# Performance work log

Hardware: AMD Instinct MI355X
Metric: run time of the kernel (lower is better)

The kernel has to match this reference:

```python
import jax, jax.numpy as jnp
import numpy as np

N_EMBED = 512
HEAD = 64
N_HEADS = N_EMBED // HEAD  # 8
N_LAYERS = 6
BLOCK = 2048
B = 4
T = 2048
SCALE = N_LAYERS / 3 ** (-0.25)  # = n_layers * 3**0.25, applied to q,k,v and FFN output


def setup_inputs() -> dict:
    key = jax.random.key(0)
    ks = jax.random.split(key, 8)
    sd = 1.0 / np.sqrt(N_EMBED)
    return {
        "x": jax.random.normal(ks[0], (B, T, N_EMBED), jnp.float32),
        "wq": jax.random.normal(ks[1], (N_HEADS, N_EMBED, HEAD), jnp.float32) * sd,
        "wk": jax.random.normal(ks[2], (N_HEADS, N_EMBED, HEAD), jnp.float32) * sd,
        "wv": jax.random.normal(ks[3], (N_HEADS, N_EMBED, HEAD), jnp.float32) * sd,
        "w_proj": jax.random.normal(ks[4], (N_EMBED, N_EMBED), jnp.float32) * sd,
        "b_proj": jnp.zeros((N_EMBED,), jnp.float32),
        "w1": jax.random.normal(ks[5], (N_EMBED, 4 * N_EMBED), jnp.float32) * sd,
        "b1": jnp.zeros((4 * N_EMBED,), jnp.float32),
        "w2": jax.random.normal(ks[6], (4 * N_EMBED, N_EMBED), jnp.float32) / np.sqrt(4 * N_EMBED),
        "b2": jnp.zeros((N_EMBED,), jnp.float32),
        "g1": jnp.ones((N_EMBED,), jnp.float32),
        "be1": jnp.zeros((N_EMBED,), jnp.float32),
        "g2": jnp.ones((N_EMBED,), jnp.float32),
        "be2": jnp.zeros((N_EMBED,), jnp.float32),
    }


def _layernorm(x, g, b, eps=1e-5):
    mu = jnp.mean(x, axis=-1, keepdims=True)
    var = jnp.var(x, axis=-1, keepdims=True)
    return (x - mu) * jax.lax.rsqrt(var + eps) * g + b


def _attention(x, wq, wk, wv, w_proj, b_proj):
    # x: [B,T,C]; wq/wk/wv: [H,C,D]  (vectorized over the per-head Linears)
    q = jnp.einsum("btc,hcd->bhtd", x, wq) * SCALE
    k = jnp.einsum("btc,hcd->bhtd", x, wk) * SCALE
    v = jnp.einsum("btc,hcd->bhtd", x, wv) * SCALE
    # NOTE: original scales by C**-0.5 where C = n_embed (input dim), not head_size
    wei = jnp.einsum("bhtd,bhsd->bhts", q, k) * (N_EMBED ** -0.5)
    causal = jnp.tril(jnp.ones((T, T), bool))  # tril buffer, sliced to [T,T]
    wei = jnp.where(causal, wei, -jnp.inf)
    wei = jax.nn.softmax(wei, axis=-1)
    out = jnp.einsum("bhts,bhsd->bhtd", wei, v)
    out = out.transpose(0, 2, 1, 3).reshape(x.shape)  # concat heads on last dim
    return out @ w_proj + b_proj


def _feedforward(x, w1, b1, w2, b2):
    h = jax.nn.relu(x @ w1 + b1)
    return (h @ w2 + b2) * SCALE


def reference(x, wq, wk, wv, w_proj, b_proj, w1, b1, w2, b2, g1, be1, g2, be2):
    x = x + _attention(_layernorm(x, g1, be1), wq, wk, wv, w_proj, b_proj)
    x = x + _feedforward(_layernorm(x, g2, be2), w1, b1, w2, b2)
    return x
```

## Files before the change

kernel.cpp:

```cpp
#include <hip/hip_runtime.h>

typedef _Float16 f16;
typedef f16 f16x4 __attribute__((ext_vector_type(4)));
typedef f16 f16x8 __attribute__((ext_vector_type(8)));
typedef float f32x4 __attribute__((ext_vector_type(4)));

#define AS1 __attribute__((address_space(1)))
#define AS3 __attribute__((address_space(3)))

constexpr float kScale  = 7.896444077714954f;
constexpr float kScaleQ = (float)(7.896444077714954 / 22.627416997969522 * 1.4426950408889634);

__device__ __forceinline__ void g2l16(const void* g, void* l) {
  __builtin_amdgcn_global_load_lds((const AS1 void*)g, (AS3 void*)l, 16, 0, 0);
}

__device__ __forceinline__ void ln_body(
    const float* __restrict__ x, const float* __restrict__ g,
    const float* __restrict__ be, f16* __restrict__ out, int rowblk) {
  int row = rowblk * 4 + ((int)threadIdx.x >> 6);
  int lane = threadIdx.x & 63;
  const float* xr = x + (size_t)row * 512;
  float xa[8];
  *(float4*)&xa[0] = *(const float4*)(xr + lane * 8);
  *(float4*)&xa[4] = *(const float4*)(xr + lane * 8 + 4);
  float s = 0.f, q = 0.f;
#pragma unroll
  for (int i = 0; i < 8; ++i) { s += xa[i]; q += xa[i] * xa[i]; }
#pragma unroll
  for (int off = 32; off; off >>= 1) { s += __shfl_xor(s, off); q += __shfl_xor(q, off); }
  float mean = s * (1.f / 512.f);
  float var = q * (1.f / 512.f) - mean * mean;
  float rstd = rsqrtf(var + 1e-5f);
  float ga[8], ba[8];
  *(float4*)&ga[0] = *(const float4*)(g + lane * 8);
  *(float4*)&ga[4] = *(const float4*)(g + lane * 8 + 4);
  *(float4*)&ba[0] = *(const float4*)(be + lane * 8);
  *(float4*)&ba[4] = *(const float4*)(be + lane * 8 + 4);
  f16x8 o;
#pragma unroll
  for (int i = 0; i < 8; ++i) o[i] = (f16)((xa[i] - mean) * rstd * ga[i] + ba[i]);
  *(f16x8*)(out + (size_t)row * 512 + lane * 8) = o;
}

__global__ __launch_bounds__(256) void ln_kernel(
    const float* __restrict__ x, const float* __restrict__ g,
    const float* __restrict__ be, f16* __restrict__ out) {
  ln_body(x, g, be, out, blockIdx.x);
}

__global__ __launch_bounds__(256) void preproc_kernel(
    const float* __restrict__ wq, const float* __restrict__ wk,
    const float* __restrict__ wv, const float* __restrict__ wp,
    const float* __restrict__ w1, const float* __restrict__ w2,
    const float* __restrict__ x, const float* __restrict__ g1,
    const float* __restrict__ be1,
    f16* __restrict__ Wqkv, f16* __restrict__ Wp, f16* __restrict__ W1t,
    f16* __restrict__ W2t, f16* __restrict__ x_ln) {
  int bid = blockIdx.x;
  if (bid >= 3072) { ln_body(x, g1, be1, x_ln, bid - 3072); return; }
  __shared__ float t[32][33];
  const float* in; f16* out; int R, Cc, bx, by, bz = 0; float scale;
  if (bid < 768) {
    int which = bid >> 8, rem = bid & 255;
    bx = rem & 1; by = (rem >> 1) & 15; bz = rem >> 5;
    in = which == 0 ? wq : (which == 1 ? wk : wv);
    out = Wqkv + (size_t)which * 512 * 512;
    R = 512; Cc = 64; scale = which == 0 ? kScaleQ : kScale;
  } else if (bid < 1024) {
    int rem = bid - 768; bx = rem & 15; by = rem >> 4;
    in = wp; out = Wp; R = 512; Cc = 512; scale = 1.f;
  } else if (bid < 2048) {
    int rem = bid - 1024; bx = rem & 63; by = rem >> 6;
    in = w1; out = W1t; R = 512; Cc = 2048; scale = 1.f;
  } else {
    int rem = bid - 2048; bx = rem & 15; by = rem >> 4;
    in = w2; out = W2t; R = 2048; Cc = 512; scale = kScale;
  }
  const float* im = in + (size_t)bz * R * Cc;
  f16* om = out + (size_t)bz * Cc * R;
  int c0 = bx * 32, r0 = by * 32;
  int tx = threadIdx.x & 31, ty = threadIdx.x >> 5;
#pragma unroll
  for (int i = 0; i < 4; ++i) {
    int rr = ty + i * 8;
    t[rr][tx] = im[(size_t)(r0 + rr) * Cc + c0 + tx] * scale;
  }
  __syncthreads();
#pragma unroll
  for (int i = 0; i < 4; ++i) {
    int rr = ty + i * 8;
    om[(size_t)(c0 + rr) * R + r0 + tx] = (f16)t[tx][rr];
  }
}

template <int MODE, bool W8>
__global__ __launch_bounds__(W8 ? 512 : 256) void gemm_bt(
    const f16* __restrict__ A, const f16* __restrict__ Bt,
    const float* __restrict__ bias, const float* __restrict__ res,
    float* __restrict__ outf, f16* __restrict__ outb,
    f16* __restrict__ qo, f16* __restrict__ ko, f16* __restrict__ vo,
    int N, int K) {
  __shared__ f16 lA[2][128 * 64], lB[2][128 * 64];
  constexpr int NF = W8 ? 2 : 4;
  constexpr int WCW = W8 ? 32 : 64;
  int tid = threadIdx.x;
  int lane = tid & 63, w = tid >> 6;
  int wr = W8 ? (w >> 2) : (w >> 1);
  int wc = W8 ? (w & 3) : (w & 1);
  int gq = lane >> 4, r = lane & 15;
  int m0 = blockIdx.x * 128, n0 = blockIdx.y * 128;
  size_t Kb = (size_t)K * 2;
  const char* Ab = (const char*)A + (size_t)m0 * Kb;
  const char* Bb = (const char*)Bt + (size_t)n0 * Kb;
  f32x4 acc[4][NF] = {};
  int srow = lane >> 3, sslot = lane & 7;
  auto stage = [&](int buf, int kt) {
#pragma unroll
    for (int i = 0; i < (W8 ? 2 : 4); ++i) {
      int chunk = i * (W8 ? 8 : 4) + w;
      int row = chunk * 8 + srow;
      int slot = sslot ^ (row & 7);
      g2l16(Ab + (size_t)row * Kb + kt * 2 + slot * 16, (char*)lA + buf * 16384 + chunk * 1024);
      g2l16(Bb + (size_t)row * Kb + kt * 2 + slot * 16, (char*)lB + buf * 16384 + chunk * 1024);
    }
  };
  stage(0, 0);
  int cur = 0;
  for (int kt = 0; kt < K; kt += 64) {
    __syncthreads();
    if (kt + 64 < K) stage(cur ^ 1, kt + 64);
    const char* bA = (const char*)lA + cur * 16384;
    const char* bB = (const char*)lB + cur * 16384;
    f16x8 af[4][2], bfr[NF][2];
#pragma unroll
    for (int f = 0; f < 4; ++f)
#pragma unroll
      for (int ks = 0; ks < 2; ++ks) {
        int ra = wr * 64 + f * 16 + r;
        af[f][ks] = *(const f16x8*)(bA + ra * 128 + (((ks * 4 + gq) ^ (ra & 7)) * 16));
      }
#pragma unroll
    for (int fn = 0; fn < NF; ++fn)
#pragma unroll
      for (int ks = 0; ks < 2; ++ks) {
        int rb = wc * WCW + fn * 16 + r;
        bfr[fn][ks] = *(const f16x8*)(bB + rb * 128 + (((ks * 4 + gq) ^ (rb & 7)) * 16));
      }
    __builtin_amdgcn_s_setprio(1);
#pragma unroll
    for (int fm = 0; fm < 4; ++fm)
#pragma unroll
      for (int fn = 0; fn < NF; ++fn)
#pragma unroll
        for (int ks = 0; ks < 2; ++ks)
          acc[fm][fn] = __builtin_amdgcn_mfma_f32_16x16x32_f16(af[fm][ks], bfr[fn][ks], acc[fm][fn], 0, 0, 0);
    __builtin_amdgcn_s_setprio(0);
    cur ^= 1;
  }
#pragma unroll
  for (int fm = 0; fm < 4; ++fm)
#pragma unroll
    for (int fn = 0; fn < NF; ++fn)
#pragma unroll
      for (int rg = 0; rg < 4; ++rg) {
        int row = m0 + wr * 64 + fm * 16 + gq * 4 + rg;
        int col = n0 + wc * WCW + fn * 16 + r;
        float v = acc[fm][fn][rg];
        if constexpr (MODE == 1) {
          outf[(size_t)row * N + col] = v + bias[col] + res[(size_t)row * N + col];
        } else if constexpr (MODE == 2) {
          outb[(size_t)row * N + col] = (f16)fmaxf(v + bias[col], 0.f);
        } else if constexpr (MODE == 3) {
          outf[(size_t)row * N + col] = v + bias[col] * kScale + res[(size_t)row * N + col];
        } else {
          int bb = row >> 11, t = row & 2047;
          int which = col >> 9, hd = col & 511, hh = hd >> 6, d = hd & 63;
          size_t bh = (size_t)bb * 8 + hh;
          if (which == 0)      qo[(bh * 2048 + t) * 64 + d] = (f16)v;
          else if (which == 1) ko[(bh * 2048 + t) * 64 + d] = (f16)v;
          else                 vo[(bh * 64 + d) * 2048 + t] = (f16)v;
        }
      }
}

__global__ __launch_bounds__(256) void attn_kernel(
    const f16* __restrict__ Q, const f16* __restrict__ K,
    const f16* __restrict__ Vt, f16* __restrict__ out) {
  __shared__ f16 lK[2][64 * 64], lV[2][64 * 64];
  __shared__ f16 lP[4][16 * 72];
  int tid = threadIdx.x, lane = tid & 63, w = tid >> 6;
  int gq = lane >> 4, r = lane & 15;
  int bh = blockIdx.x;
  int p = blockIdx.y;
  const char* Qb = (const char*)(Q + (size_t)bh * 2048 * 64);
  const char* Kb = (const char*)(K + (size_t)bh * 2048 * 64);
  const char* Vb = (const char*)(Vt + (size_t)bh * 64 * 2048);
  int q0A = p * 64 + w * 16;
  int q0B = (31 - p) * 64 + w * 16;
  f16x8 qfA[2], qfB[2];
#pragma unroll
  for (int ks = 0; ks < 2; ++ks) {
    qfA[ks] = *(const f16x8*)(Qb + (size_t)(q0A + r) * 128 + ks * 64 + gq * 16);
    qfB[ks] = *(const f16x8*)(Qb + (size_t)(q0B + r) * 128 + ks * 64 + gq * 16);
  }
  f16x8 ones;
#pragma unroll
  for (int i = 0; i < 8; ++i) ones[i] = (f16)1.f;
  f32x4 OA[4] = {}, OB[4] = {}, OlA = {}, OlB = {};
  float mA = -1e30f, mB = -1e30f;
  int srow = lane >> 3, sslot = lane & 7;

  auto stage = [&](int buf, int kv) {
    int j0 = kv * 64;
#pragma unroll
    for (int i = 0; i < 2; ++i) {
      int chunk = i * 4 + w;
      int row = chunk * 8 + srow;
      int slot = sslot ^ (row & 7);
      g2l16(Kb + (size_t)(j0 + row) * 128 + slot * 16, (char*)lK + buf * 8192 + chunk * 1024);
      g2l16(Vb + (size_t)row * 4096 + j0 * 2 + slot * 16, (char*)lV + buf * 8192 + chunk * 1024);
    }
  };

  f16x8 vf[4][2];
  auto smpv = [&](f32x4 (&s)[4], float& m, f32x4 (&O)[4], f32x4& Ol) {
    float t0 = fmaxf(fmaxf(s[0][0], s[0][1]), fmaxf(s[0][2], s[0][3]));
    float t1 = fmaxf(fmaxf(s[1][0], s[1][1]), fmaxf(s[1][2], s[1][3]));
    float t2 = fmaxf(fmaxf(s[2][0], s[2][1]), fmaxf(s[2][2], s[2][3]));
    float t3 = fmaxf(fmaxf(s[3][0], s[3][1]), fmaxf(s[3][2], s[3][3]));
    float pmax = fmaxf(fmaxf(t0, t1), fmaxf(t2, t3));
    pmax = fmaxf(pmax, __shfl_xor(pmax, 16));
    pmax = fmaxf(pmax, __shfl_xor(pmax, 32));
    float mn = fmaxf(m, pmax);
    if (mn - m > 11.5f) {
      float sc = exp2f(m - mn);
#pragma unroll
      for (int fd = 0; fd < 4; ++fd) O[fd] *= sc;
      Ol *= sc;
      m = mn;
    } else {
      mn = m;
    }
#pragma unroll
    for (int fc = 0; fc < 4; ++fc) {
      f16x4 pv;
#pragma unroll
      for (int rg = 0; rg < 4; ++rg) pv[rg] = (f16)exp2f(s[fc][rg] - mn);
      *(f16x4*)((char*)&lP[w][0] + r * 144 + fc * 32 + gq * 8) = pv;
    }
    f16x8 pf[2];
#pragma unroll
    for (int ks = 0; ks < 2; ++ks)
      pf[ks] = *(const f16x8*)((const char*)&lP[w][0] + r * 144 + ks * 64 + gq * 16);
#pragma unroll
    for (int fd = 0; fd < 4; ++fd)
#pragma unroll
      for (int ks = 0; ks < 2; ++ks)
        O[fd] = __builtin_amdgcn_mfma_f32_16x16x32_f16(vf[fd][ks], pf[ks], O[fd], 0, 0, 0);
#pragma unroll
    for (int ks = 0; ks < 2; ++ks)
      Ol = __builtin_amdgcn_mfma_f32_16x16x32_f16(ones, pf[ks], Ol, 0, 0, 0);
  };

  int nkv = 32 - p;
  stage(0, 0);
  int cur = 0;
  for (int kv = 0; kv < nkv; ++kv) {
    int j0 = kv * 64;
    __syncthreads();
    if (kv + 1 < nkv) stage(cur ^ 1, kv + 1);
    const char* bK = (const char*)lK + cur * 8192;
    const char* bV = (const char*)lV + cur * 8192;
    f16x8 kf[4][2];
#pragma unroll
    for (int fc = 0; fc < 4; ++fc)
#pragma unroll
      for (int ks = 0; ks < 2; ++ks) {
        int rj = fc * 16 + r;
        kf[fc][ks] = *(const f16x8*)(bK + rj * 128 + (((ks * 4 + gq) ^ (rj & 7)) * 16));
      }
#pragma unroll
    for (int fd = 0; fd < 4; ++fd)
#pragma unroll
      for (int ks = 0; ks < 2; ++ks) {
        int rd = fd * 16 + r;
        vf[fd][ks] = *(const f16x8*)(bV + rd * 128 + (((ks * 4 + gq) ^ (rd & 7)) * 16));
      }
    f32x4 sB[4] = {};
#pragma unroll
    for (int ks = 0; ks < 2; ++ks)
#pragma unroll
      for (int fc = 0; fc < 4; ++fc)
        sB[fc] = __builtin_amdgcn_mfma_f32_16x16x32_f16(kf[fc][ks], qfB[ks], sB[fc], 0, 0, 0);
    if (kv == nkv - 1) {
      int t = q0B + r;
#pragma unroll
      for (int fc = 0; fc < 4; ++fc)
#pragma unroll
        for (int rg = 0; rg < 4; ++rg) {
          int j = j0 + fc * 16 + gq * 4 + rg;
          if (j > t) sB[fc][rg] = -1e30f;
        }
    }
    smpv(sB, mB, OB, OlB);
    if (kv <= p) {
      f32x4 sA[4] = {};
#pragma unroll
      for (int ks = 0; ks < 2; ++ks)
#pragma unroll
        for (int fc = 0; fc < 4; ++fc)
          sA[fc] = __builtin_amdgcn_mfma_f32_16x16x32_f16(kf[fc][ks], qfA[ks], sA[fc], 0, 0, 0);
      if (kv == p) {
        int t = q0A + r;
#pragma unroll
        for (int fc = 0; fc < 4; ++fc)
#pragma unroll
          for (int rg = 0; rg < 4; ++rg) {
            int j = j0 + fc * 16 + gq * 4 + rg;
            if (j > t) sA[fc][rg] = -1e30f;
          }
      }
      smpv(sA, mA, OA, OlA);
    }
    cur ^= 1;
  }
  int bb = bh >> 3, hh = bh & 7;
  auto wout = [&](int q0, f32x4 (&O)[4], float l) {
    float inv = 1.f / l;
    int t = q0 + r;
    f16* o = out + ((size_t)bb * 2048 + t) * 512 + hh * 64 + gq * 4;
#pragma unroll
    for (int fd = 0; fd < 4; ++fd) {
      f16x4 v;
#pragma unroll
      for (int rg = 0; rg < 4; ++rg) v[rg] = (f16)(O[fd][rg] * inv);
      *(f16x4*)(o + fd * 16) = v;
    }
  };
  wout(q0A, OA, OlA[0]);
  wout(q0B, OB, OlB[0]);
}

extern "C" void kernel_launch(void* const* d_in, const int* in_sizes, int n_in,
                              void* d_out, int out_size, void* d_ws, size_t ws_size,
                              hipStream_t stream) {
  (void)in_sizes; (void)n_in; (void)out_size; (void)ws_size;
  const float* x      = (const float*)d_in[0];
  const float* wq     = (const float*)d_in[1];
  const float* wk     = (const float*)d_in[2];
  const float* wv     = (const float*)d_in[3];
  const float* w_proj = (const float*)d_in[4];
  const float* b_proj = (const float*)d_in[5];
  const float* w1     = (const float*)d_in[6];
  const float* b1     = (const float*)d_in[7];
  const float* w2     = (const float*)d_in[8];
  const float* b2     = (const float*)d_in[9];
  const float* g1     = (const float*)d_in[10];
  const float* be1    = (const float*)d_in[11];
  const float* g2     = (const float*)d_in[12];
  const float* be2    = (const float*)d_in[13];
  float* outp = (float*)d_out;

  char* ws = (char*)d_ws;
  size_t off = 0;
  auto alloc = [&](size_t bytes) {
    char* p = ws + off;
    off += (bytes + 255) & ~(size_t)255;
    return p;
  };
  const size_t MC2 = (size_t)8192 * 512 * 2;
  f16* x_ln  = (f16*)alloc(MC2);
  f16* qb    = (f16*)alloc(MC2);
  f16* kb    = (f16*)alloc(MC2);
  f16* vb    = (f16*)alloc(MC2);
  f16* attn  = (f16*)alloc(MC2);
  float* x1  = (float*)alloc((size_t)8192 * 512 * 4);
  f16* Wqkv  = (f16*)alloc((size_t)1536 * 512 * 2);
  f16* Wp    = (f16*)alloc((size_t)512 * 512 * 2);
  f16* W1t   = (f16*)alloc((size_t)2048 * 512 * 2);
  f16* W2t   = (f16*)alloc((size_t)512 * 2048 * 2);
  f16* x1_ln = x_ln;
  f16* hbuf  = qb;

  preproc_kernel<<<5120, 256, 0, stream>>>(wq, wk, wv, w_proj, w1, w2, x, g1, be1,
                                           Wqkv, Wp, W1t, W2t, x_ln);
  gemm_bt<0, false><<<dim3(64, 12), 256, 0, stream>>>(x_ln, Wqkv, nullptr, nullptr, nullptr, nullptr,
                                                      qb, kb, vb, 1536, 512);
  attn_kernel<<<dim3(32, 16), 256, 0, stream>>>(qb, kb, vb, attn);
  gemm_bt<1, true><<<dim3(64, 4), 512, 0, stream>>>(attn, Wp, b_proj, x, x1, nullptr,
                                                    nullptr, nullptr, nullptr, 512, 512);
  ln_kernel<<<2048, 256, 0, stream>>>(x1, g2, be2, x1_ln);
  gemm_bt<2, false><<<dim3(64, 16), 256, 0, stream>>>(x1_ln, W1t, b1, nullptr, nullptr, hbuf,
                                                      nullptr, nullptr, nullptr, 2048, 512);
  gemm_bt<3, true><<<dim3(64, 4), 512, 0, stream>>>(hbuf, W2t, b2, x1, outp, nullptr,
                                                    nullptr, nullptr, nullptr, 512, 2048);
}
```

Baseline: 165.9 us.

## Replace paired causal query tiles with one query tile per block, heaviest first

Measured after the change: 163.1 us. Within noise of the previous version (-1.7%).

```diff
diff --git a/kernel.cpp b/kernel.cpp
--- a/kernel.cpp
+++ b/kernel.cpp
@@ -192,23 +192,20 @@
   int tid = threadIdx.x, lane = tid & 63, w = tid >> 6;
   int gq = lane >> 4, r = lane & 15;
   int bh = blockIdx.x;
-  int p = blockIdx.y;
+  int qt = 31 - (int)blockIdx.y;
   const char* Qb = (const char*)(Q + (size_t)bh * 2048 * 64);
   const char* Kb = (const char*)(K + (size_t)bh * 2048 * 64);
   const char* Vb = (const char*)(Vt + (size_t)bh * 64 * 2048);
-  int q0A = p * 64 + w * 16;
-  int q0B = (31 - p) * 64 + w * 16;
-  f16x8 qfA[2], qfB[2];
-#pragma unroll
-  for (int ks = 0; ks < 2; ++ks) {
-    qfA[ks] = *(const f16x8*)(Qb + (size_t)(q0A + r) * 128 + ks * 64 + gq * 16);
-    qfB[ks] = *(const f16x8*)(Qb + (size_t)(q0B + r) * 128 + ks * 64 + gq * 16);
-  }
+  int q0 = qt * 64 + w * 16;
+  f16x8 qf[2];
+#pragma unroll
+  for (int ks = 0; ks < 2; ++ks)
+    qf[ks] = *(const f16x8*)(Qb + (size_t)(q0 + r) * 128 + ks * 64 + gq * 16);
   f16x8 ones;
 #pragma unroll
   for (int i = 0; i < 8; ++i) ones[i] = (f16)1.f;
-  f32x4 OA[4] = {}, OB[4] = {}, OlA = {}, OlB = {};
-  float mA = -1e30f, mB = -1e30f;
+  f32x4 O[4] = {}, Ol = {};
+  float m = -1e30f;
   int srow = lane >> 3, sslot = lane & 7;
 
   auto stage = [&](int buf, int kv) {
@@ -223,8 +220,41 @@
     }
   };
 
-  f16x8 vf[4][2];
-  auto smpv = [&](f32x4 (&s)[4], float& m, f32x4 (&O)[4], f32x4& Ol) {
+  int nkv = qt + 1;
+  stage(0, 0);
+  int cur = 0;
+  for (int kv = 0; kv < nkv; ++kv) {
+    int j0 = kv * 64;
+    __syncthreads();
+    if (kv + 1 < nkv) stage(cur ^ 1, kv + 1);
+    const char* bK = (const char*)lK + cur * 8192;
+    const char* bV = (const char*)lV + cur * 8192;
+    f16x8 kf[4][2], vf[4][2];
+#pragma unroll
+    for (int fc = 0; fc < 4; ++fc)
+#pragma unroll
+      for (int ks = 0; ks < 2; ++ks) {
+        int rj = fc * 16 + r;
+        int off = rj * 128 + (((ks * 4 + gq) ^ (rj & 7)) * 16);
+        kf[fc][ks] = *(const f16x8*)(bK + off);
+        vf[fc][ks] = *(const f16x8*)(bV + off);
+      }
+    f32x4 s[4] = {};
+#pragma unroll
+    for (int ks = 0; ks < 2; ++ks)
+#pragma unroll
+      for (int fc = 0; fc < 4; ++fc)
+        s[fc] = __builtin_amdgcn_mfma_f32_16x16x32_f16(kf[fc][ks], qf[ks], s[fc], 0, 0, 0);
+    if (kv == qt) {
+      int t = q0 + r;
+#pragma unroll
+      for (int fc = 0; fc < 4; ++fc)
+#pragma unroll
+        for (int rg = 0; rg < 4; ++rg) {
+          int j = j0 + fc * 16 + gq * 4 + rg;
+          if (j > t) s[fc][rg] = -1e30f;
+        }
+    }
     float t0 = fmaxf(fmaxf(s[0][0], s[0][1]), fmaxf(s[0][2], s[0][3]));
     float t1 = fmaxf(fmaxf(s[1][0], s[1][1]), fmaxf(s[1][2], s[1][3]));
     float t2 = fmaxf(fmaxf(s[2][0], s[2][1]), fmaxf(s[2][2], s[2][3]));
@@ -261,85 +291,19 @@
 #pragma unroll
     for (int ks = 0; ks < 2; ++ks)
       Ol = __builtin_amdgcn_mfma_f32_16x16x32_f16(ones, pf[ks], Ol, 0, 0, 0);
-  };
-
-  int nkv = 32 - p;
-  stage(0, 0);
-  int cur = 0;
-  for (int kv = 0; kv < nkv; ++kv) {
-    int j0 = kv * 64;
-    __syncthreads();
-    if (kv + 1 < nkv) stage(cur ^ 1, kv + 1);
-    const char* bK = (const char*)lK + cur * 8192;
-    const char* bV = (const char*)lV + cur * 8192;
-    f16x8 kf[4][2];
-#pragma unroll
-    for (int fc = 0; fc < 4; ++fc)
-#pragma unroll
-      for (int ks = 0; ks < 2; ++ks) {
-        int rj = fc * 16 + r;
-        kf[fc][ks] = *(const f16x8*)(bK + rj * 128 + (((ks * 4 + gq) ^ (rj & 7)) * 16));
-      }
-#pragma unroll
-    for (int fd = 0; fd < 4; ++fd)
-#pragma unroll
-      for (int ks = 0; ks < 2; ++ks) {
-        int rd = fd * 16 + r;
-        vf[fd][ks] = *(const f16x8*)(bV + rd * 128 + (((ks * 4 + gq) ^ (rd & 7)) * 16));
-      }
-    f32x4 sB[4] = {};
-#pragma unroll
-    for (int ks = 0; ks < 2; ++ks)
-#pragma unroll
-      for (int fc = 0; fc < 4; ++fc)
-        sB[fc] = __builtin_amdgcn_mfma_f32_16x16x32_f16(kf[fc][ks], qfB[ks], sB[fc], 0, 0, 0);
-    if (kv == nkv - 1) {
-      int t = q0B + r;
-#pragma unroll
-      for (int fc = 0; fc < 4; ++fc)
-#pragma unroll
-        for (int rg = 0; rg < 4; ++rg) {
-          int j = j0 + fc * 16 + gq * 4 + rg;
-          if (j > t) sB[fc][rg] = -1e30f;
-        }
-    }
-    smpv(sB, mB, OB, OlB);
-    if (kv <= p) {
-      f32x4 sA[4] = {};
-#pragma unroll
-      for (int ks = 0; ks < 2; ++ks)
-#pragma unroll
-        for (int fc = 0; fc < 4; ++fc)
-          sA[fc] = __builtin_amdgcn_mfma_f32_16x16x32_f16(kf[fc][ks], qfA[ks], sA[fc], 0, 0, 0);
-      if (kv == p) {
-        int t = q0A + r;
-#pragma unroll
-        for (int fc = 0; fc < 4; ++fc)
-#pragma unroll
-          for (int rg = 0; rg < 4; ++rg) {
-            int j = j0 + fc * 16 + gq * 4 + rg;
-            if (j > t) sA[fc][rg] = -1e30f;
-          }
-      }
-      smpv(sA, mA, OA, OlA);
-    }
     cur ^= 1;
   }
   int bb = bh >> 3, hh = bh & 7;
-  auto wout = [&](int q0, f32x4 (&O)[4], float l) {
-    float inv = 1.f / l;
-    int t = q0 + r;
-    f16* o = out + ((size_t)bb * 2048 + t) * 512 + hh * 64 + gq * 4;
-#pragma unroll
-    for (int fd = 0; fd < 4; ++fd) {
-      f16x4 v;
-#pragma unroll
-      for (int rg = 0; rg < 4; ++rg) v[rg] = (f16)(O[fd][rg] * inv);
-      *(f16x4*)(o + fd * 16) = v;
-    }
-  };
-  wout(q0A, OA, OlA[0]);
-  wout(q0B, OB, OlB[0]);
+  float inv = 1.f / Ol[0];
+  int t = q0 + r;
+  f16* o = out + ((size_t)bb * 2048 + t) * 512 + hh * 64 + gq * 4;
+#pragma unroll
+  for (int fd = 0; fd < 4; ++fd) {
+    f16x4 v;
+#pragma unroll
+    for (int rg = 0; rg < 4; ++rg) v[rg] = (f16)(O[fd][rg] * inv);
+    *(f16x4*)(o + fd * 16) = v;
+  }
 }
 
 extern "C" void kernel_launch(void* const* d_in, const int* in_sizes, int n_in,
@@ -387,7 +351,7 @@
                                            Wqkv, Wp, W1t, W2t, x_ln);
   gemm_bt<0, false><<<dim3(64, 12), 256, 0, stream>>>(x_ln, Wqkv, nullptr, nullptr, nullptr, nullptr,
                                                       qb, kb, vb, 1536, 512);
-  attn_kernel<<<dim3(32, 16), 256, 0, stream>>>(qb, kb, vb, attn);
+  attn_kernel<<<dim3(32, 32), 256, 0, stream>>>(qb, kb, vb, attn);
   gemm_bt<1, true><<<dim3(64, 4), 512, 0, stream>>>(attn, Wp, b_proj, x, x1, nullptr,
                                                     nullptr, nullptr, nullptr, 512, 512);
   ln_kernel<<<2048, 256, 0, stream>>>(x1, g2, be2, x1_ln);
```

## Pair adjacent query tiles per block, fold running max into MFMA accumulator init

Applied to the files above, without the earlier changes.

Result: slower. 185.3 us (+11.7%).

```diff
diff --git a/kernel.cpp b/kernel.cpp
--- a/kernel.cpp
+++ b/kernel.cpp
@@ -3,6 +3,7 @@
 typedef _Float16 f16;
 typedef f16 f16x4 __attribute__((ext_vector_type(4)));
 typedef f16 f16x8 __attribute__((ext_vector_type(8)));
+typedef __fp16 h16x2 __attribute__((ext_vector_type(2)));
 typedef float f32x4 __attribute__((ext_vector_type(4)));
 
 #define AS1 __attribute__((address_space(1)))
@@ -188,16 +189,17 @@
     const f16* __restrict__ Q, const f16* __restrict__ K,
     const f16* __restrict__ Vt, f16* __restrict__ out) {
   __shared__ f16 lK[2][64 * 64], lV[2][64 * 64];
-  __shared__ f16 lP[4][16 * 72];
+  __shared__ f16 lP[4][2][16 * 64];
   int tid = threadIdx.x, lane = tid & 63, w = tid >> 6;
   int gq = lane >> 4, r = lane & 15;
   int bh = blockIdx.x;
-  int p = blockIdx.y;
+  int qt = 15 - (int)blockIdx.y;
   const char* Qb = (const char*)(Q + (size_t)bh * 2048 * 64);
   const char* Kb = (const char*)(K + (size_t)bh * 2048 * 64);
   const char* Vb = (const char*)(Vt + (size_t)bh * 64 * 2048);
-  int q0A = p * 64 + w * 16;
-  int q0B = (31 - p) * 64 + w * 16;
+  int q0A = qt * 128 + w * 16;
+  int q0B = q0A + 64;
+  int dgA = 2 * qt, dgB = 2 * qt + 1;
   f16x8 qfA[2], qfB[2];
 #pragma unroll
   for (int ks = 0; ks < 2; ++ks) {
@@ -210,6 +212,7 @@
   f32x4 OA[4] = {}, OB[4] = {}, OlA = {}, OlB = {};
   float mA = -1e30f, mB = -1e30f;
   int srow = lane >> 3, sslot = lane & 7;
+  int swz = (r & 7) << 4;
 
   auto stage = [&](int buf, int kv) {
     int j0 = kv * 64;
@@ -223,36 +226,40 @@
     }
   };
 
-  f16x8 vf[4][2];
-  auto smpv = [&](f32x4 (&s)[4], float& m, f32x4 (&O)[4], f32x4& Ol) {
-    float t0 = fmaxf(fmaxf(s[0][0], s[0][1]), fmaxf(s[0][2], s[0][3]));
-    float t1 = fmaxf(fmaxf(s[1][0], s[1][1]), fmaxf(s[1][2], s[1][3]));
-    float t2 = fmaxf(fmaxf(s[2][0], s[2][1]), fmaxf(s[2][2], s[2][3]));
-    float t3 = fmaxf(fmaxf(s[3][0], s[3][1]), fmaxf(s[3][2], s[3][3]));
-    float pmax = fmaxf(fmaxf(t0, t1), fmaxf(t2, t3));
+  f16x8 kf[4][2], vf[4][2];
+  auto smpv = [&](f32x4 (&s)[4], float& m, f32x4 (&O)[4], f32x4& Ol, char* lPw) {
+    float pmax = s[0][0];
+#pragma unroll
+    for (int fc = 0; fc < 4; ++fc)
+#pragma unroll
+      for (int rg = 0; rg < 4; ++rg)
+        if (fc + rg) pmax = fmaxf(pmax, s[fc][rg]);
     pmax = fmaxf(pmax, __shfl_xor(pmax, 16));
     pmax = fmaxf(pmax, __shfl_xor(pmax, 32));
-    float mn = fmaxf(m, pmax);
-    if (mn - m > 11.5f) {
-      float sc = exp2f(m - mn);
+    if (pmax > 11.5f || m < -1e29f) {
+      float sc = exp2f(-pmax);
 #pragma unroll
       for (int fd = 0; fd < 4; ++fd) O[fd] *= sc;
       Ol *= sc;
-      m = mn;
-    } else {
-      mn = m;
+      m = (m < -1e29f) ? pmax : m + pmax;
+#pragma unroll
+      for (int fc = 0; fc < 4; ++fc)
+#pragma unroll
+        for (int rg = 0; rg < 4; ++rg) s[fc][rg] -= pmax;
     }
 #pragma unroll
     for (int fc = 0; fc < 4; ++fc) {
+      h16x2 p01 = __builtin_amdgcn_cvt_pkrtz(exp2f(s[fc][0]), exp2f(s[fc][1]));
+      h16x2 p23 = __builtin_amdgcn_cvt_pkrtz(exp2f(s[fc][2]), exp2f(s[fc][3]));
       f16x4 pv;
-#pragma unroll
-      for (int rg = 0; rg < 4; ++rg) pv[rg] = (f16)exp2f(s[fc][rg] - mn);
-      *(f16x4*)((char*)&lP[w][0] + r * 144 + fc * 32 + gq * 8) = pv;
+      *(h16x2*)&pv = p01;
+      *((h16x2*)&pv + 1) = p23;
+      *(f16x4*)(lPw + r * 128 + ((fc * 32 + gq * 8) ^ swz)) = pv;
     }
     f16x8 pf[2];
 #pragma unroll
     for (int ks = 0; ks < 2; ++ks)
-      pf[ks] = *(const f16x8*)((const char*)&lP[w][0] + r * 144 + ks * 64 + gq * 16);
+      pf[ks] = *(const f16x8*)(lPw + r * 128 + ((ks * 64 + gq * 16) ^ swz));
 #pragma unroll
     for (int fd = 0; fd < 4; ++fd)
 #pragma unroll
@@ -263,7 +270,7 @@
       Ol = __builtin_amdgcn_mfma_f32_16x16x32_f16(ones, pf[ks], Ol, 0, 0, 0);
   };
 
-  int nkv = 32 - p;
+  int nkv = 2 * qt + 2;
   stage(0, 0);
   int cur = 0;
   for (int kv = 0; kv < nkv; ++kv) {
@@ -272,46 +279,27 @@
     if (kv + 1 < nkv) stage(cur ^ 1, kv + 1);
     const char* bK = (const char*)lK + cur * 8192;
     const char* bV = (const char*)lV + cur * 8192;
-    f16x8 kf[4][2];
 #pragma unroll
     for (int fc = 0; fc < 4; ++fc)
 #pragma unroll
       for (int ks = 0; ks < 2; ++ks) {
         int rj = fc * 16 + r;
-        kf[fc][ks] = *(const f16x8*)(bK + rj * 128 + (((ks * 4 + gq) ^ (rj & 7)) * 16));
-      }
-#pragma unroll
-    for (int fd = 0; fd < 4; ++fd)
-#pragma unroll
-      for (int ks = 0; ks < 2; ++ks) {
-        int rd = fd * 16 + r;
-        vf[fd][ks] = *(const f16x8*)(bV + rd * 128 + (((ks * 4 + gq) ^ (rd & 7)) * 16));
-      }
-    f32x4 sB[4] = {};
-#pragma unroll
-    for (int ks = 0; ks < 2; ++ks)
-#pragma unroll
-      for (int fc = 0; fc < 4; ++fc)
-        sB[fc] = __builtin_amdgcn_mfma_f32_16x16x32_f16(kf[fc][ks], qfB[ks], sB[fc], 0, 0, 0);
-    if (kv == nkv - 1) {
-      int t = q0B + r;
-#pragma unroll
-      for (int fc = 0; fc < 4; ++fc)
-#pragma unroll
-        for (int rg = 0; rg < 4; ++rg) {
-          int j = j0 + fc * 16 + gq * 4 + rg;
-          if (j > t) sB[fc][rg] = -1e30f;
-        }
-    }
-    smpv(sB, mB, OB, OlB);
-    if (kv <= p) {
-      f32x4 sA[4] = {};
+        int off = rj * 128 + (((ks * 4 + gq) ^ (rj & 7)) * 16);
+        kf[fc][ks] = *(const f16x8*)(bK + off);
+        vf[fc][ks] = *(const f16x8*)(bV + off);
+      }
+    bool actA = (kv <= dgA);
+    if (actA) {
+      float bias = (mA > -1e29f) ? -mA : 0.f;
+      f32x4 sA[4];
+#pragma unroll
+      for (int fc = 0; fc < 4; ++fc) sA[fc] = f32x4{bias, bias, bias, bias};
 #pragma unroll
       for (int ks = 0; ks < 2; ++ks)
 #pragma unroll
         for (int fc = 0; fc < 4; ++fc)
           sA[fc] = __builtin_amdgcn_mfma_f32_16x16x32_f16(kf[fc][ks], qfA[ks], sA[fc], 0, 0, 0);
-      if (kv == p) {
+      if (kv == dgA) {
         int t = q0A + r;
 #pragma unroll
         for (int fc = 0; fc < 4; ++fc)
@@ -321,7 +309,29 @@
             if (j > t) sA[fc][rg] = -1e30f;
           }
       }
-      smpv(sA, mA, OA, OlA);
+      smpv(sA, mA, OA, OlA, (char*)&lP[w][0][0]);
+    }
+    {
+      float bias = (mB > -1e29f) ? -mB : 0.f;
+      f32x4 sB[4];
+#pragma unroll
+      for (int fc = 0; fc < 4; ++fc) sB[fc] = f32x4{bias, bias, bias, bias};
+#pragma unroll
+      for (int ks = 0; ks < 2; ++ks)
+#pragma unroll
+        for (int fc = 0; fc < 4; ++fc)
+          sB[fc] = __builtin_amdgcn_mfma_f32_16x16x32_f16(kf[fc][ks], qfB[ks], sB[fc], 0, 0, 0);
+      if (kv == dgB) {
+        int t = q0B + r;
+#pragma unroll
+        for (int fc = 0; fc < 4; ++fc)
+#pragma unroll
+          for (int rg = 0; rg < 4; ++rg) {
+            int j = j0 + fc * 16 + gq * 4 + rg;
+            if (j > t) sB[fc][rg] = -1e30f;
+          }
+      }
+      smpv(sB, mB, OB, OlB, (char*)&lP[w][1][0]);
     }
     cur ^= 1;
   }
```
